# Optimization experiments

Measured on AMD Instinct MI355X. Metric: run time of the kernel, lower is better.

## Reference

```python
import jax, jax.numpy as jnp
import numpy as np
from jax.ops import segment_sum

N_NODES = 50000
N_EDGES = 150000
IN_FEATS = 512
OUT_FEATS = 512


def setup_inputs() -> dict:
    key = jax.random.key(0)
    k1, k2, k3, k4 = jax.random.split(key, 4)
    x = jax.random.normal(k1, (N_NODES, IN_FEATS), dtype=jnp.float32)
    src = jax.random.randint(k2, (N_EDGES,), 0, N_NODES, dtype=jnp.int64)
    dst = jax.random.randint(k3, (N_EDGES,), 0, N_NODES, dtype=jnp.int64)
    # Xavier-uniform init like reset_parameters
    limit = float(np.sqrt(6.0 / (IN_FEATS + OUT_FEATS)))
    W = jax.random.uniform(k4, (IN_FEATS, OUT_FEATS), dtype=jnp.float32,
                           minval=-limit, maxval=limit)
    b = jnp.zeros((OUT_FEATS,), dtype=jnp.float32)
    return {"x": x, "src": src, "dst": dst, "W": W, "b": b}


def reference(x, src, dst, W, b):
    # DGL GraphConv with norm='both':
    #   out = relu( D_dst^{-1/2} A D_src^{-1/2} X W + b )
    # Dropout is identity in eval mode (training=False).
    ones = jnp.ones((src.shape[0],), dtype=x.dtype)
    deg_out = segment_sum(ones, src, num_segments=N_NODES)  # source out-degree
    deg_in = segment_sum(ones, dst, num_segments=N_NODES)   # dest in-degree
    norm_src = jnp.where(deg_out > 0, deg_out, 1.0) ** -0.5  # [N]
    norm_dst = jnp.where(deg_in > 0, deg_in, 1.0) ** -0.5    # [N]

    h = x * norm_src[:, None]                         # [N, in]
    agg = segment_sum(h[src], dst, num_segments=N_NODES)  # scatter-add over edges
    agg = agg * norm_dst[:, None]                     # [N, in]
    out = agg @ W + b                                 # [N, out]
    return jax.nn.relu(out)
```

## Files before the change

kernel.cpp:

```cpp
#include <hip/hip_runtime.h>
#include <hip/hip_bf16.h>

#define N_NODES 50000
#define N_PAD   50048
#define N_EDGES 150000
#define F 512
#define BM 128
#define BN 128
#define BK 64
#define NBLK 196
#define NWG  1564

typedef __attribute__((ext_vector_type(4))) float f32x4;
typedef __attribute__((ext_vector_type(4))) unsigned int u32x4;
typedef __attribute__((ext_vector_type(2))) unsigned int u32x2;

__device__ __forceinline__ unsigned short f2bf(float f) {
    unsigned int u = __float_as_uint(f);
    return (unsigned short)((u + 0x7fffu + ((u >> 16) & 1u)) >> 16);
}
__device__ __forceinline__ unsigned int pack2(float a, float b) {
    return (unsigned int)f2bf(a) | ((unsigned int)f2bf(b) << 16);
}
__device__ __forceinline__ void gload16(const void* g, void* l) {
    __builtin_amdgcn_global_load_lds(
        (const __attribute__((address_space(1))) unsigned int*)g,
        (__attribute__((address_space(3))) unsigned int*)l, 16, 0, 0);
}

__global__ void __launch_bounds__(256) crd_deg(const int* __restrict__ src,
                                               const int* __restrict__ dst,
                                               int* __restrict__ hist) {
    int e = blockIdx.x * 256 + threadIdx.x;
    if (e < N_EDGES) {
        atomicAdd(&hist[src[e]], 1);
        atomicAdd(&hist[N_NODES + dst[e]], 1);
    }
}

__global__ void __launch_bounds__(256) crd_norm(const int* __restrict__ hist,
                                                float* __restrict__ norms) {
    int i = blockIdx.x * 256 + threadIdx.x;
    if (i < 2 * N_NODES) {
        int d = hist[i];
        norms[i] = rsqrtf((float)(d > 0 ? d : 1));
    }
}

__global__ void __launch_bounds__(256) crd_bsum(const int* __restrict__ hist_in,
                                                int* __restrict__ bsum) {
    __shared__ int s[256];
    int t = threadIdx.x;
    int i = blockIdx.x * 256 + t;
    s[t] = (i < N_NODES) ? hist_in[i] : 0;
    __syncthreads();
    #pragma unroll
    for (int o = 128; o > 0; o >>= 1) {
        if (t < o) s[t] += s[t + o];
        __syncthreads();
    }
    if (t == 0) bsum[blockIdx.x] = s[0];
}

__global__ void __launch_bounds__(256) crd_bscan(const int* __restrict__ bsum,
                                                 int* __restrict__ bsumoff) {
    __shared__ int s[256];
    int t = threadIdx.x;
    int v = (t < NBLK) ? bsum[t] : 0;
    s[t] = v;
    __syncthreads();
    #pragma unroll
    for (int d = 1; d < 256; d <<= 1) {
        int add = (t >= d) ? s[t - d] : 0;
        __syncthreads();
        s[t] += add;
        __syncthreads();
    }
    if (t < NBLK) bsumoff[t] = s[t] - v;
}

__global__ void __launch_bounds__(256) crd_escan(const int* __restrict__ hist_in,
                                                 const int* __restrict__ bsumoff,
                                                 int* __restrict__ off,
                                                 int* __restrict__ cursor) {
    __shared__ int s[256];
    int t = threadIdx.x;
    int i = blockIdx.x * 256 + t;
    int v = (i < N_NODES) ? hist_in[i] : 0;
    s[t] = v;
    __syncthreads();
    #pragma unroll
    for (int d = 1; d < 256; d <<= 1) {
        int add = (t >= d) ? s[t - d] : 0;
        __syncthreads();
        s[t] += add;
        __syncthreads();
    }
    int excl = s[t] - v + bsumoff[blockIdx.x];
    if (i < N_NODES) { off[i] = excl; cursor[i] = excl; }
    if (i == N_NODES - 1) off[N_NODES] = excl + v;
}

__global__ void __launch_bounds__(256) crd_place(const int* __restrict__ src,
                                                 const int* __restrict__ dst,
                                                 int* __restrict__ cursor,
                                                 int* __restrict__ sorted) {
    int e = blockIdx.x * 256 + threadIdx.x;
    if (e < N_EDGES) {
        int slot = atomicAdd(&cursor[dst[e]], 1);
        sorted[slot] = src[e];
    }
}

__global__ void __launch_bounds__(256) crd_wt(const float* __restrict__ W,
                                              unsigned short* __restrict__ Wt) {
    int idx = blockIdx.x * 256 + threadIdx.x;
    int n = idx >> 9, k = idx & 511;
    Wt[idx] = f2bf(W[k * F + n]);
}

__global__ void __launch_bounds__(256) crd_xb(const float* __restrict__ x,
                                              const float* __restrict__ norms,
                                              unsigned short* __restrict__ xb) {
    int t = blockIdx.x * 256 + threadIdx.x;
    size_t i = (size_t)t * 8;
    float ns = norms[t >> 6];
    f32x4 v0 = *(const f32x4*)(x + i);
    f32x4 v1 = *(const f32x4*)(x + i + 4);
    v0 *= ns; v1 *= ns;
    u32x4 w;
    w.x = pack2(v0.x, v0.y); w.y = pack2(v0.z, v0.w);
    w.z = pack2(v1.x, v1.y); w.w = pack2(v1.z, v1.w);
    *(u32x4*)(xb + i) = w;
}

__device__ __forceinline__ void acc8(float* a, u32x4 v) {
    a[0] += __uint_as_float(v.x << 16); a[1] += __uint_as_float(v.x & 0xffff0000u);
    a[2] += __uint_as_float(v.y << 16); a[3] += __uint_as_float(v.y & 0xffff0000u);
    a[4] += __uint_as_float(v.z << 16); a[5] += __uint_as_float(v.z & 0xffff0000u);
    a[6] += __uint_as_float(v.w << 16); a[7] += __uint_as_float(v.w & 0xffff0000u);
}

__global__ void __launch_bounds__(256) crd_gather_bf(const unsigned short* __restrict__ xb,
                                                     const int* __restrict__ sorted,
                                                     const int* __restrict__ off,
                                                     const float* __restrict__ norms,
                                                     unsigned short* __restrict__ aggb) {
    int wid = (blockIdx.x * 256 + threadIdx.x) >> 6;
    int lane = threadIdx.x & 63;
    if (wid >= N_PAD) return;
    float a[8] = {0.f,0.f,0.f,0.f,0.f,0.f,0.f,0.f};
    float b[8] = {0.f,0.f,0.f,0.f,0.f,0.f,0.f,0.f};
    if (wid < N_NODES) {
        int e0 = off[wid], e1 = off[wid + 1];
        int e = e0;
        for (; e + 1 < e1; e += 2) {
            int s0 = sorted[e], s1 = sorted[e + 1];
            u32x4 v0 = *(const u32x4*)(xb + (size_t)s0 * F + lane * 8);
            u32x4 v1 = *(const u32x4*)(xb + (size_t)s1 * F + lane * 8);
            acc8(a, v0);
            acc8(b, v1);
        }
        if (e < e1) {
            u32x4 v0 = *(const u32x4*)(xb + (size_t)sorted[e] * F + lane * 8);
            acc8(a, v0);
        }
        float nd = norms[N_NODES + wid];
        #pragma unroll
        for (int j = 0; j < 8; ++j) a[j] = (a[j] + b[j]) * nd;
    }
    u32x4 w;
    w.x = pack2(a[0], a[1]); w.y = pack2(a[2], a[3]);
    w.z = pack2(a[4], a[5]); w.w = pack2(a[6], a[7]);
    *(u32x4*)(aggb + (size_t)wid * F + lane * 8) = w;
}

__global__ void __launch_bounds__(256) crd_gather_f32(const float* __restrict__ x,
                                                      const int* __restrict__ sorted,
                                                      const int* __restrict__ off,
                                                      const float* __restrict__ norms,
                                                      unsigned short* __restrict__ aggb) {
    int wid = (blockIdx.x * 256 + threadIdx.x) >> 6;
    int lane = threadIdx.x & 63;
    if (wid >= N_PAD) return;
    f32x4 a0 = {0.f,0.f,0.f,0.f}, a1 = a0;
    if (wid < N_NODES) {
        int e0 = off[wid], e1 = off[wid + 1];
        for (int e = e0; e < e1; ++e) {
            int s = sorted[e];
            float ns = norms[s];
            const f32x4* p = (const f32x4*)(x + (size_t)s * F);
            a0 += p[lane] * ns;
            a1 += p[64 + lane] * ns;
        }
        float nd = norms[N_NODES + wid];
        a0 *= nd; a1 *= nd;
    }
    unsigned short* row = aggb + (size_t)wid * F;
    u32x2 w0, w1;
    w0.x = pack2(a0.x, a0.y); w0.y = pack2(a0.z, a0.w);
    w1.x = pack2(a1.x, a1.y); w1.y = pack2(a1.z, a1.w);
    *(u32x2*)(row + lane * 4) = w0;
    *(u32x2*)(row + 256 + lane * 4) = w1;
}

__global__ void __launch_bounds__(256, 2) crd_gemm(const unsigned short* __restrict__ aggb,
                                                   const unsigned short* __restrict__ Wt,
                                                   const float* __restrict__ bias,
                                                   float* __restrict__ out) {
    __shared__ __align__(16) unsigned short lA[2][8 * BM * 8];
    __shared__ __align__(16) unsigned short lB[2][8 * BN * 8];
    const int tid = threadIdx.x;
    int bid = blockIdx.x;
    int xcd = bid & 7, lid = bid >> 3;
    int swz = (xcd < 4 ? xcd * 196 : 784 + (xcd - 4) * 195) + lid;
    const int rowbase = (swz >> 2) * BM;
    const int nbase = (swz & 3) * BN;
    const int lane = tid & 63;
    const int wave = tid >> 6;
    const int wm = wave >> 1, wn = wave & 1;
    const int g = lane >> 4, r = lane & 15;

    f32x4 zero4 = {0.f, 0.f, 0.f, 0.f};
    f32x4 acc[4][4];
    #pragma unroll
    for (int i = 0; i < 4; ++i)
        #pragma unroll
        for (int j = 0; j < 4; ++j) acc[i][j] = zero4;

#define STAGE(B, KS) do { \
    _Pragma("unroll") \
    for (int j_ = 0; j_ < 4; ++j_) { \
        int gg = (wave * 4 + j_) * 64 + lane; \
        int k8 = gg >> 7, rw = gg & 127; \
        gload16(aggb + (size_t)(rowbase + rw) * F + (KS) * BK + k8 * 8, \
                &lA[B][(wave * 4 + j_) * 512]); \
    } \
    _Pragma("unroll") \
    for (int j_ = 0; j_ < 4; ++j_) { \
        int gg = (wave * 4 + j_) * 64 + lane; \
        int k8 = gg >> 7, nn = gg & 127; \
        gload16(Wt + (size_t)(nbase + nn) * F + (KS) * BK + k8 * 8, \
                &lB[B][(wave * 4 + j_) * 512]); \
    } \
} while (0)

#define COMPUTE(B) do { \
    _Pragma("unroll") \
    for (int kk = 0; kk < 2; ++kk) { \
        int k8 = kk * 4 + g; \
        u32x4 af[4], bfr[4]; \
        _Pragma("unroll") \
        for (int mi = 0; mi < 4; ++mi) \
            af[mi] = *(const u32x4*)&lA[B][(k8 * BM + wm * 64 + mi * 16 + r) * 8]; \
        _Pragma("unroll") \
        for (int ni = 0; ni < 4; ++ni) \
            bfr[ni] = *(const u32x4*)&lB[B][(k8 * BN + wn * 64 + ni * 16 + r) * 8]; \
        _Pragma("unroll") \
        for (int mi = 0; mi < 4; ++mi) \
            _Pragma("unroll") \
            for (int ni = 0; ni < 4; ++ni) \
                asm("v_mfma_f32_16x16x32_bf16 %0, %1, %2, %0" \
                    : "+v"(acc[mi][ni]) : "v"(af[mi]), "v"(bfr[ni])); \
    } \
} while (0)

    STAGE(0, 0);
    __syncthreads();
    #pragma unroll
    for (int ks2 = 0; ks2 < 4; ++ks2) {
        STAGE(1, 2 * ks2 + 1);
        COMPUTE(0);
        __syncthreads();
        if (ks2 < 3) STAGE(0, 2 * ks2 + 2);
        COMPUTE(1);
        __syncthreads();
    }
#undef STAGE
#undef COMPUTE

    #pragma unroll
    for (int ni = 0; ni < 4; ++ni) {
        int col = nbase + wn * 64 + ni * 16 + r;
        float bv = bias[col];
        #pragma unroll
        for (int mi = 0; mi < 4; ++mi) {
            #pragma unroll
            for (int j = 0; j < 4; ++j) {
                int row = rowbase + wm * 64 + mi * 16 + g * 4 + j;
                if (row < N_NODES) {
                    float v = acc[mi][ni][j] + bv;
                    out[(size_t)row * F + col] = v > 0.0f ? v : 0.0f;
                }
            }
        }
    }
}

extern "C" void kernel_launch(void* const* d_in, const int* in_sizes, int n_in,
                              void* d_out, int out_size, void* d_ws, size_t ws_size,
                              hipStream_t stream) {
    const float* x = (const float*)d_in[0];
    const int* src = (const int*)d_in[1];
    const int* dst = (const int*)d_in[2];
    const float* W = (const float*)d_in[3];
    const float* bias = (const float*)d_in[4];
    float* out = (float*)d_out;

    unsigned short* aggb = (unsigned short*)d_ws;
    unsigned short* Wt = aggb + (size_t)N_PAD * F;
    float* norms = (float*)(Wt + (size_t)F * F);
    int* hist = (int*)(norms + 2 * N_NODES);
    int* off = hist + 2 * N_NODES;
    int* cursor = off + N_NODES + 1;
    int* sorted = cursor + N_NODES;
    int* bsum = sorted + N_EDGES;
    int* bsumoff = bsum + NBLK;
    char* endp = (char*)(bsumoff + NBLK);
    unsigned short* xb = (unsigned short*)(((uintptr_t)endp + 63) & ~(uintptr_t)63);
    size_t need_min = (size_t)(endp - (char*)d_ws);
    size_t need_bf = (size_t)((char*)(xb + (size_t)N_NODES * F) - (char*)d_ws);
    if (ws_size < need_min) {
        hipMemsetAsync(d_out, 0, (size_t)out_size * sizeof(float), stream);
        return;
    }
    const bool use_bf = (ws_size >= need_bf);

    hipMemsetAsync(hist, 0, 2 * N_NODES * sizeof(int), stream);
    crd_deg<<<(N_EDGES + 255) / 256, 256, 0, stream>>>(src, dst, hist);
    crd_norm<<<(2 * N_NODES + 255) / 256, 256, 0, stream>>>(hist, norms);
    crd_bsum<<<NBLK, 256, 0, stream>>>(hist + N_NODES, bsum);
    crd_bscan<<<1, 256, 0, stream>>>(bsum, bsumoff);
    crd_escan<<<NBLK, 256, 0, stream>>>(hist + N_NODES, bsumoff, off, cursor);
    crd_wt<<<(F * F) / 256, 256, 0, stream>>>(W, Wt);
    crd_place<<<(N_EDGES + 255) / 256, 256, 0, stream>>>(src, dst, cursor, sorted);
    if (use_bf) {
        crd_xb<<<(int)(((size_t)N_NODES * F / 8) / 256), 256, 0, stream>>>(x, norms, xb);
        crd_gather_bf<<<N_PAD / 4, 256, 0, stream>>>(xb, sorted, off, norms, aggb);
    } else {
        crd_gather_f32<<<N_PAD / 4, 256, 0, stream>>>(x, sorted, off, norms, aggb);
    }
    crd_gemm<<<NWG, 256, 0, stream>>>(aggb, Wt, bias, out);
}
```

Before: 196.1 us.

## Make GEMM persistent with W slice resident in LDS and streamed A tiles

Replaces the 1564-workgroup tiled GEMM with 256 persistent 512-thread workgroups. Each workgroup loads its full 128-column slice of bf16 Wt (128 KB) into LDS once, then loops over 6-7 row tiles, streaming A in 32-wide K chunks through a triple buffer with explicit vmcnt waits and a barrier per step. The aim is to stop re-reading W for every tile and to cut launch and prologue overhead. In exchange, the very large LDS footprint limits occupancy to one workgroup per CU, and the smaller per-wave tile (32x64) with a barrier every K step may leave the MFMA units underfed.

```diff
diff --git a/kernel.cpp b/kernel.cpp
--- a/kernel.cpp
+++ b/kernel.cpp
@@ -5,11 +5,8 @@
 #define N_PAD   50048
 #define N_EDGES 150000
 #define F 512
-#define BM 128
 #define BN 128
-#define BK 64
 #define NBLK 196
-#define NWG  1564
 
 typedef __attribute__((ext_vector_type(4))) float f32x4;
 typedef __attribute__((ext_vector_type(4))) unsigned int u32x4;
@@ -204,93 +201,96 @@
     *(u32x2*)(row + 256 + lane * 4) = w1;
 }
 
-__global__ void __launch_bounds__(256, 2) crd_gemm(const unsigned short* __restrict__ aggb,
+__global__ void __launch_bounds__(512, 2) crd_gemm(const unsigned short* __restrict__ aggb,
                                                    const unsigned short* __restrict__ Wt,
                                                    const float* __restrict__ bias,
                                                    float* __restrict__ out) {
-    __shared__ __align__(16) unsigned short lA[2][8 * BM * 8];
-    __shared__ __align__(16) unsigned short lB[2][8 * BN * 8];
+    __shared__ __align__(16) unsigned short lB[64 * 128 * 8];
+    __shared__ __align__(16) unsigned short lA[3][4 * 128 * 8];
     const int tid = threadIdx.x;
-    int bid = blockIdx.x;
-    int xcd = bid & 7, lid = bid >> 3;
-    int swz = (xcd < 4 ? xcd * 196 : 784 + (xcd - 4) * 195) + lid;
-    const int rowbase = (swz >> 2) * BM;
-    const int nbase = (swz & 3) * BN;
-    const int lane = tid & 63;
-    const int wave = tid >> 6;
-    const int wm = wave >> 1, wn = wave & 1;
+    const int wave = tid >> 6, lane = tid & 63;
     const int g = lane >> 4, r = lane & 15;
-
-    f32x4 zero4 = {0.f, 0.f, 0.f, 0.f};
-    f32x4 acc[4][4];
-    #pragma unroll
-    for (int i = 0; i < 4; ++i)
+    const int wm = wave >> 1;
+    const int wn = wave & 1;
+    const int nbase = (blockIdx.x & 3) * BN;
+    const int mgrp = blockIdx.x >> 2;
+    const int njobs = (mgrp < 7) ? 7 : 6;
+    const int total = njobs * 16;
+
+    #pragma unroll
+    for (int j = 0; j < 16; ++j) {
+        int gg = j * 512 + tid;
+        int k8g = gg >> 7, n = gg & 127;
+        gload16(Wt + (size_t)(nbase + n) * F + k8g * 8,
+                &lB[(size_t)(j * 512 + wave * 64) * 8]);
+    }
+    {
+        int k8 = tid >> 7, rw = tid & 127;
+        const unsigned short* p = aggb + (size_t)(mgrp * 128 + rw) * F + k8 * 8;
+        gload16(p, &lA[0][wave * 512]);
+        gload16(p + 32, &lA[1][wave * 512]);
+    }
+    float bv[4];
+    #pragma unroll
+    for (int ni = 0; ni < 4; ++ni) bv[ni] = bias[nbase + wn * 64 + ni * 16 + r];
+
+    __syncthreads();
+
+    f32x4 acc[2][4];
+    #pragma unroll
+    for (int mi = 0; mi < 2; ++mi)
         #pragma unroll
-        for (int j = 0; j < 4; ++j) acc[i][j] = zero4;
-
-#define STAGE(B, KS) do { \
-    _Pragma("unroll") \
-    for (int j_ = 0; j_ < 4; ++j_) { \
-        int gg = (wave * 4 + j_) * 64 + lane; \
-        int k8 = gg >> 7, rw = gg & 127; \
-        gload16(aggb + (size_t)(rowbase + rw) * F + (KS) * BK + k8 * 8, \
-                &lA[B][(wave * 4 + j_) * 512]); \
-    } \
-    _Pragma("unroll") \
-    for (int j_ = 0; j_ < 4; ++j_) { \
-        int gg = (wave * 4 + j_) * 64 + lane; \
-        int k8 = gg >> 7, nn = gg & 127; \
-        gload16(Wt + (size_t)(nbase + nn) * F + (KS) * BK + k8 * 8, \
-                &lB[B][(wave * 4 + j_) * 512]); \
-    } \
-} while (0)
-
-#define COMPUTE(B) do { \
-    _Pragma("unroll") \
-    for (int kk = 0; kk < 2; ++kk) { \
-        int k8 = kk * 4 + g; \
-        u32x4 af[4], bfr[4]; \
-        _Pragma("unroll") \
-        for (int mi = 0; mi < 4; ++mi) \
-            af[mi] = *(const u32x4*)&lA[B][(k8 * BM + wm * 64 + mi * 16 + r) * 8]; \
-        _Pragma("unroll") \
-        for (int ni = 0; ni < 4; ++ni) \
-            bfr[ni] = *(const u32x4*)&lB[B][(k8 * BN + wn * 64 + ni * 16 + r) * 8]; \
-        _Pragma("unroll") \
-        for (int mi = 0; mi < 4; ++mi) \
-            _Pragma("unroll") \
-            for (int ni = 0; ni < 4; ++ni) \
-                asm("v_mfma_f32_16x16x32_bf16 %0, %1, %2, %0" \
-                    : "+v"(acc[mi][ni]) : "v"(af[mi]), "v"(bfr[ni])); \
-    } \
-} while (0)
-
-    STAGE(0, 0);
-    __syncthreads();
-    #pragma unroll
-    for (int ks2 = 0; ks2 < 4; ++ks2) {
-        STAGE(1, 2 * ks2 + 1);
-        COMPUTE(0);
-        __syncthreads();
-        if (ks2 < 3) STAGE(0, 2 * ks2 + 2);
-        COMPUTE(1);
-        __syncthreads();
-    }
-#undef STAGE
-#undef COMPUTE
-
-    #pragma unroll
-    for (int ni = 0; ni < 4; ++ni) {
-        int col = nbase + wn * 64 + ni * 16 + r;
-        float bv = bias[col];
-        #pragma unroll
-        for (int mi = 0; mi < 4; ++mi) {
+        for (int ni = 0; ni < 4; ++ni) acc[mi][ni] = (f32x4){0.f, 0.f, 0.f, 0.f};
+
+    for (int s = 0; s < total; ++s) {
+        int ks = s & 15;
+        if (s + 2 < total) {
+            int s2 = s + 2;
+            int rb2 = (mgrp + ((s2 >> 4) << 6)) * 128;
+            int ks2 = s2 & 15;
+            int k8 = tid >> 7, rw = tid & 127;
+            gload16(aggb + (size_t)(rb2 + rw) * F + ks2 * 32 + k8 * 8,
+                    &lA[s2 % 3][wave * 512]);
+        }
+        {
+            const unsigned short* la = lA[s % 3];
+            int k8g = ks * 4 + g;
+            u32x4 af0 = *(const u32x4*)&la[(g * 128 + wm * 32 + r) * 8];
+            u32x4 af1 = *(const u32x4*)&la[(g * 128 + wm * 32 + 16 + r) * 8];
+            u32x4 bf0 = *(const u32x4*)&lB[(size_t)(k8g * 128 + wn * 64 + r) * 8];
+            u32x4 bf1 = *(const u32x4*)&lB[(size_t)(k8g * 128 + wn * 64 + 16 + r) * 8];
+            u32x4 bf2 = *(const u32x4*)&lB[(size_t)(k8g * 128 + wn * 64 + 32 + r) * 8];
+            u32x4 bf3 = *(const u32x4*)&lB[(size_t)(k8g * 128 + wn * 64 + 48 + r) * 8];
+            asm("v_mfma_f32_16x16x32_bf16 %0, %1, %2, %0" : "+v"(acc[0][0]) : "v"(af0), "v"(bf0));
+            asm("v_mfma_f32_16x16x32_bf16 %0, %1, %2, %0" : "+v"(acc[0][1]) : "v"(af0), "v"(bf1));
+            asm("v_mfma_f32_16x16x32_bf16 %0, %1, %2, %0" : "+v"(acc[0][2]) : "v"(af0), "v"(bf2));
+            asm("v_mfma_f32_16x16x32_bf16 %0, %1, %2, %0" : "+v"(acc[0][3]) : "v"(af0), "v"(bf3));
+            asm("v_mfma_f32_16x16x32_bf16 %0, %1, %2, %0" : "+v"(acc[1][0]) : "v"(af1), "v"(bf0));
+            asm("v_mfma_f32_16x16x32_bf16 %0, %1, %2, %0" : "+v"(acc[1][1]) : "v"(af1), "v"(bf1));
+            asm("v_mfma_f32_16x16x32_bf16 %0, %1, %2, %0" : "+v"(acc[1][2]) : "v"(af1), "v"(bf2));
+            asm("v_mfma_f32_16x16x32_bf16 %0, %1, %2, %0" : "+v"(acc[1][3]) : "v"(af1), "v"(bf3));
+        }
+        if (s + 2 < total) asm volatile("s_waitcnt vmcnt(1)" ::: "memory");
+        else               asm volatile("s_waitcnt vmcnt(0)" ::: "memory");
+        __builtin_amdgcn_s_barrier();
+        asm volatile("" ::: "memory");
+
+        if (ks == 15) {
+            int rowb = (mgrp + ((s >> 4) << 6)) * 128 + wm * 32;
             #pragma unroll
-            for (int j = 0; j < 4; ++j) {
-                int row = rowbase + wm * 64 + mi * 16 + g * 4 + j;
-                if (row < N_NODES) {
-                    float v = acc[mi][ni][j] + bv;
-                    out[(size_t)row * F + col] = v > 0.0f ? v : 0.0f;
+            for (int ni = 0; ni < 4; ++ni) {
+                int col = nbase + wn * 64 + ni * 16 + r;
+                #pragma unroll
+                for (int mi = 0; mi < 2; ++mi) {
+                    #pragma unroll
+                    for (int jj = 0; jj < 4; ++jj) {
+                        int row = rowb + mi * 16 + g * 4 + jj;
+                        if (row < N_NODES) {
+                            float v = acc[mi][ni][jj] + bv[ni];
+                            out[(size_t)row * F + col] = v > 0.0f ? v : 0.0f;
+                        }
+                        acc[mi][ni][jj] = 0.0f;
+                    }
                 }
             }
         }
@@ -340,5 +340,5 @@
     } else {
         crd_gather_f32<<<N_PAD / 4, 256, 0, stream>>>(x, sorted, off, norms, aggb);
     }
-    crd_gemm<<<NWG, 256, 0, stream>>>(aggb, Wt, bias, out);
-}
+    crd_gemm<<<256, 512, 0, stream>>>(aggb, Wt, bias, out);
+}
```

Measured after the change: 182.3 us. -7.0%, faster.

## Load GEMM MFMA operands directly from global memory, dropping LDS staging

Applied to the files above, without the earlier changes.

The GEMM kernel no longer stages A and B tiles through double-buffered LDS with global_load_lds and barriers. Each lane now reads its MFMA fragments straight from global memory (or cache) in a fully unrolled 16-step K loop. This removes the LDS traffic and the __syncthreads barriers, but it loses intra-workgroup operand sharing, so each wave refetches the A/B data it needs through L1/L2. It also drops the occupancy hint of 2 from the launch bounds.

```diff
diff --git a/kernel.cpp b/kernel.cpp
--- a/kernel.cpp
+++ b/kernel.cpp
@@ -5,9 +5,6 @@
 #define N_PAD   50048
 #define N_EDGES 150000
 #define F 512
-#define BM 128
-#define BN 128
-#define BK 64
 #define NBLK 196
 #define NWG  1564
 
@@ -21,11 +18,6 @@
 }
 __device__ __forceinline__ unsigned int pack2(float a, float b) {
     return (unsigned int)f2bf(a) | ((unsigned int)f2bf(b) << 16);
-}
-__device__ __forceinline__ void gload16(const void* g, void* l) {
-    __builtin_amdgcn_global_load_lds(
-        (const __attribute__((address_space(1))) unsigned int*)g,
-        (__attribute__((address_space(3))) unsigned int*)l, 16, 0, 0);
 }
 
 __global__ void __launch_bounds__(256) crd_deg(const int* __restrict__ src,
@@ -204,80 +196,51 @@
     *(u32x2*)(row + 256 + lane * 4) = w1;
 }
 
-__global__ void __launch_bounds__(256, 2) crd_gemm(const unsigned short* __restrict__ aggb,
-                                                   const unsigned short* __restrict__ Wt,
-                                                   const float* __restrict__ bias,
-                                                   float* __restrict__ out) {
-    __shared__ __align__(16) unsigned short lA[2][8 * BM * 8];
-    __shared__ __align__(16) unsigned short lB[2][8 * BN * 8];
+__global__ void __launch_bounds__(256) crd_gemm(const unsigned short* __restrict__ aggb,
+                                                const unsigned short* __restrict__ Wt,
+                                                const float* __restrict__ bias,
+                                                float* __restrict__ out) {
     const int tid = threadIdx.x;
-    int bid = blockIdx.x;
-    int xcd = bid & 7, lid = bid >> 3;
-    int swz = (xcd < 4 ? xcd * 196 : 784 + (xcd - 4) * 195) + lid;
-    const int rowbase = (swz >> 2) * BM;
-    const int nbase = (swz & 3) * BN;
     const int lane = tid & 63;
     const int wave = tid >> 6;
     const int wm = wave >> 1, wn = wave & 1;
     const int g = lane >> 4, r = lane & 15;
 
-    f32x4 zero4 = {0.f, 0.f, 0.f, 0.f};
+    int bid = blockIdx.x;
+    int xcd = bid & 7, lid = bid >> 3;
+    int swz = (xcd < 4 ? xcd * 196 : 784 + (xcd - 4) * 195) + lid;
+    const int rowbase = (swz >> 2) * 128;
+    const int nbase = (swz & 3) * 128;
+
+    const unsigned short* pa[4];
+    const unsigned short* pb[4];
+    #pragma unroll
+    for (int mi = 0; mi < 4; ++mi)
+        pa[mi] = aggb + (size_t)(rowbase + wm * 64 + mi * 16 + r) * F + g * 8;
+    #pragma unroll
+    for (int ni = 0; ni < 4; ++ni)
+        pb[ni] = Wt + (size_t)(nbase + wn * 64 + ni * 16 + r) * F + g * 8;
+
     f32x4 acc[4][4];
     #pragma unroll
     for (int i = 0; i < 4; ++i)
         #pragma unroll
-        for (int j = 0; j < 4; ++j) acc[i][j] = zero4;
-
-#define STAGE(B, KS) do { \
-    _Pragma("unroll") \
-    for (int j_ = 0; j_ < 4; ++j_) { \
-        int gg = (wave * 4 + j_) * 64 + lane; \
-        int k8 = gg >> 7, rw = gg & 127; \
-        gload16(aggb + (size_t)(rowbase + rw) * F + (KS) * BK + k8 * 8, \
-                &lA[B][(wave * 4 + j_) * 512]); \
-    } \
-    _Pragma("unroll") \
-    for (int j_ = 0; j_ < 4; ++j_) { \
-        int gg = (wave * 4 + j_) * 64 + lane; \
-        int k8 = gg >> 7, nn = gg & 127; \
-        gload16(Wt + (size_t)(nbase + nn) * F + (KS) * BK + k8 * 8, \
-                &lB[B][(wave * 4 + j_) * 512]); \
-    } \
-} while (0)
-
-#define COMPUTE(B) do { \
-    _Pragma("unroll") \
-    for (int kk = 0; kk < 2; ++kk) { \
-        int k8 = kk * 4 + g; \
-        u32x4 af[4], bfr[4]; \
-        _Pragma("unroll") \
-        for (int mi = 0; mi < 4; ++mi) \
-            af[mi] = *(const u32x4*)&lA[B][(k8 * BM + wm * 64 + mi * 16 + r) * 8]; \
-        _Pragma("unroll") \
-        for (int ni = 0; ni < 4; ++ni) \
-            bfr[ni] = *(const u32x4*)&lB[B][(k8 * BN + wn * 64 + ni * 16 + r) * 8]; \
-        _Pragma("unroll") \
-        for (int mi = 0; mi < 4; ++mi) \
-            _Pragma("unroll") \
-            for (int ni = 0; ni < 4; ++ni) \
-                asm("v_mfma_f32_16x16x32_bf16 %0, %1, %2, %0" \
-                    : "+v"(acc[mi][ni]) : "v"(af[mi]), "v"(bfr[ni])); \
-    } \
-} while (0)
-
-    STAGE(0, 0);
-    __syncthreads();
-    #pragma unroll
-    for (int ks2 = 0; ks2 < 4; ++ks2) {
-        STAGE(1, 2 * ks2 + 1);
-        COMPUTE(0);
-        __syncthreads();
-        if (ks2 < 3) STAGE(0, 2 * ks2 + 2);
-        COMPUTE(1);
-        __syncthreads();
-    }
-#undef STAGE
-#undef COMPUTE
+        for (int j = 0; j < 4; ++j) acc[i][j] = (f32x4){0.f, 0.f, 0.f, 0.f};
+
+    #pragma unroll
+    for (int ks = 0; ks < 16; ++ks) {
+        u32x4 af[4], bf[4];
+        #pragma unroll
+        for (int mi = 0; mi < 4; ++mi) af[mi] = *(const u32x4*)(pa[mi] + ks * 32);
+        #pragma unroll
+        for (int ni = 0; ni < 4; ++ni) bf[ni] = *(const u32x4*)(pb[ni] + ks * 32);
+        #pragma unroll
+        for (int mi = 0; mi < 4; ++mi)
+            #pragma unroll
+            for (int ni = 0; ni < 4; ++ni)
+                asm("v_mfma_f32_16x16x32_bf16 %0, %1, %2, %0"
+                    : "+v"(acc[mi][ni]) : "v"(af[mi]), "v"(bf[ni]));
+    }
 
     #pragma unroll
     for (int ni = 0; ni < 4; ++ni) {
```

Result: slower. 219.5 us (+11.9%).
